# Performance work log

Measured on AMD Instinct MI355X. Metric: run time of the kernel, lower is better.

The kernel has to match this reference:

```python
import jax, jax.numpy as jnp
import numpy as np

N_NODES = 40000
N_EDGES = 1280000
D_FEAT = 1024
HIDDEN = 64
N_CLASSES = 40


def gcn_conv(x, edge_index, W, b):
    # PyG GCNConv: linear transform, add self-loops, symmetric deg^{-1/2} normalization, scatter-add
    n = x.shape[0]
    h = x @ W  # [N, out]
    loop = jnp.arange(n, dtype=edge_index.dtype)
    row = jnp.concatenate([edge_index[0], loop])  # source
    col = jnp.concatenate([edge_index[1], loop])  # target
    deg = jax.ops.segment_sum(jnp.ones_like(col, dtype=x.dtype), col, num_segments=n)
    dinv = jnp.where(deg > 0, jax.lax.rsqrt(deg), 0.0).astype(x.dtype)
    norm = dinv[row] * dinv[col]  # [E+N]
    msg = h[row] * norm[:, None]
    out = jax.ops.segment_sum(msg, col, num_segments=n)
    return out + b


def setup_inputs() -> dict:
    key = jax.random.key(0)
    k1, k2, k3, k4 = jax.random.split(key, 4)
    x = jax.random.normal(k1, (N_NODES, D_FEAT), dtype=jnp.float32)
    edge_index = jax.random.randint(k2, (2, N_EDGES), 0, N_NODES, dtype=jnp.int32)
    W1 = jax.random.normal(k3, (D_FEAT, HIDDEN), dtype=jnp.float32) * (1.0 / np.sqrt(D_FEAT))
    b1 = jnp.zeros((HIDDEN,), dtype=jnp.float32)
    W2 = jax.random.normal(k4, (HIDDEN, N_CLASSES), dtype=jnp.float32) * (1.0 / np.sqrt(HIDDEN))
    b2 = jnp.zeros((N_CLASSES,), dtype=jnp.float32)
    return {"x": x, "edge_index": edge_index, "W1": W1, "b1": b1, "W2": W2, "b2": b2}


def reference(x, edge_index, W1, b1, W2, b2):
    h = gcn_conv(x, edge_index, W1, b1)
    h = jax.nn.relu(h)
    # F.dropout(training=False) -> identity in eval mode
    h = gcn_conv(h, edge_index, W2, b2)
    return jax.nn.log_softmax(h, axis=1)
```

## Files before the change

### kernel.cpp

```cpp
#include <hip/hip_runtime.h>
#include <hip/hip_bf16.h>
#include <math.h>

#define N_NODES 40000
#define N_EDGES 1280000
#define D_FEAT 1024
#define HIDDEN 64
#define N_CLASSES 40
#define NB 157
#define CHUNK 8192

typedef _Float16 f16x8 __attribute__((ext_vector_type(8)));
typedef _Float16 f16x2 __attribute__((ext_vector_type(2)));
typedef float f32x4 __attribute__((ext_vector_type(4)));


__global__ __launch_bounds__(256) void k_binhist(const int* __restrict__ col,
                                                 int* __restrict__ btot) {
    __shared__ int h[NB];
    int tid = threadIdx.x;
    if (tid < NB) h[tid] = 0;
    __syncthreads();
    int e0 = blockIdx.x * 4096;
    int e1 = min(e0 + 4096, N_EDGES);
    for (int e = e0 + tid; e < e1; e += 256)
        atomicAdd(&h[col[e] >> 8], 1);
    __syncthreads();
    if (tid < NB && h[tid]) atomicAdd(&btot[tid], h[tid]);
}


__global__ __launch_bounds__(256) void k_bucketscan(const int* __restrict__ btot,
                                                    int* __restrict__ bucketBase,
                                                    int* __restrict__ bucketCursor) {
    __shared__ int s[256];
    int tid = threadIdx.x;
    int v = (tid < NB) ? btot[tid] : 0;
    s[tid] = v;
    __syncthreads();
#pragma unroll
    for (int d = 1; d < 256; d <<= 1) {
        int t = (tid >= d) ? s[tid - d] : 0;
        __syncthreads();
        s[tid] += t;
        __syncthreads();
    }
    int excl = s[tid] - v;
    if (tid < NB) { bucketBase[tid] = excl; bucketCursor[tid] = excl; }
    if (tid == 0) bucketBase[NB] = N_EDGES;
}


__global__ __launch_bounds__(256) void k_binscatter(const int* __restrict__ row,
                                                    const int* __restrict__ col,
                                                    int* __restrict__ bucketCursor,
                                                    uint2* __restrict__ sedge) {
    __shared__ int hist[NB];
    __shared__ int chunkBase[NB];
    __shared__ int cur[NB];
    int tid = threadIdx.x;
    int e0 = blockIdx.x * CHUNK;
    int e1 = min(e0 + CHUNK, N_EDGES);
    if (tid < NB) { hist[tid] = 0; cur[tid] = 0; }
    __syncthreads();
    for (int e = e0 + tid; e < e1; e += 256)
        atomicAdd(&hist[col[e] >> 8], 1);
    __syncthreads();
    if (tid < NB)
        chunkBase[tid] = hist[tid] ? atomicAdd(&bucketCursor[tid], hist[tid]) : 0;
    __syncthreads();
    for (int e = e0 + tid; e < e1; e += 256) {
        int c = col[e];
        int b = c >> 8;
        int p = atomicAdd(&cur[b], 1);
        sedge[chunkBase[b] + p] = make_uint2((unsigned)row[e], (unsigned)c);
    }
}


__global__ __launch_bounds__(256) void k_bucketsort(const uint2* __restrict__ sedge,
                                                    const int* __restrict__ bucketBase,
                                                    int* __restrict__ off,
                                                    float* __restrict__ dinv,
                                                    int* __restrict__ sorted) {
    __shared__ int hist[256];
    __shared__ int s[256];
    __shared__ int cur[256];
    int tid = threadIdx.x;
    int b = blockIdx.x;
    int base = bucketBase[b], end = bucketBase[b + 1];
    int col0 = b << 8;
    int ncol = min(256, N_NODES - col0);
    hist[tid] = 0;
    __syncthreads();
    for (int i = base + tid; i < end; i += 256)
        atomicAdd(&hist[sedge[i].y & 255], 1);
    __syncthreads();
    int v = hist[tid];
    s[tid] = v;
    __syncthreads();
#pragma unroll
    for (int d = 1; d < 256; d <<= 1) {
        int t = (tid >= d) ? s[tid - d] : 0;
        __syncthreads();
        s[tid] += t;
        __syncthreads();
    }
    int excl = s[tid] - v;
    cur[tid] = excl;
    if (tid < ncol) {
        off[col0 + tid] = base + excl;
        dinv[col0 + tid] = rsqrtf((float)(v + 1));
    }
    if (b == NB - 1 && tid == 0) off[N_NODES] = N_EDGES;
    __syncthreads();
    for (int i = base + tid; i < end; i += 256) {
        uint2 e = sedge[i];
        int p = atomicAdd(&cur[e.y & 255], 1);
        sorted[base + p] = (int)e.x;
    }
}


__global__ void k_convW1(const float* __restrict__ W, _Float16* __restrict__ Wt) {
    int i = blockIdx.x * 256 + threadIdx.x;
    if (i < D_FEAT * HIDDEN) {
        int n = i & 63, k = i >> 6;
        Wt[n * D_FEAT + k] = (_Float16)W[k * HIDDEN + n];
    }
}


#define LDA 72
#define LDB 72

__global__ __launch_bounds__(256) void k_gemm1(const float* __restrict__ X,
                                               const _Float16* __restrict__ Wt,
                                               const float* __restrict__ dinv,
                                               _Float16* __restrict__ out) {
    __shared__ _Float16 As[32 * LDA];
    __shared__ _Float16 Bs[64 * LDB];
    const int tid = threadIdx.x;
    const int wave = tid >> 6, lane = tid & 63;
    const int row0 = blockIdx.x * 32;
    const int m0 = (wave & 1) * 16, n0 = (wave >> 1) * 32;
    const int lr = lane & 15, quad = lane >> 4;

    const int ar = tid >> 3;
    const int ak = (tid & 7) * 8;
    const int bn = tid >> 2;
    const int bk = (tid & 3) * 16;

    f32x4 acc0 = {0.f, 0.f, 0.f, 0.f};
    f32x4 acc1 = {0.f, 0.f, 0.f, 0.f};

    for (int k0 = 0; k0 < D_FEAT; k0 += 64) {
        const float* xp = &X[(row0 + ar) * D_FEAT + k0 + ak];
        float4 v0 = *(const float4*)xp;
        float4 v1 = *(const float4*)(xp + 4);
        _Float16* ad = &As[ar * LDA + ak];
        ad[0] = (_Float16)v0.x; ad[1] = (_Float16)v0.y;
        ad[2] = (_Float16)v0.z; ad[3] = (_Float16)v0.w;
        ad[4] = (_Float16)v1.x; ad[5] = (_Float16)v1.y;
        ad[6] = (_Float16)v1.z; ad[7] = (_Float16)v1.w;
        const uint4* wp = (const uint4*)&Wt[bn * D_FEAT + k0 + bk];
        uint4 w0 = wp[0], w1 = wp[1];
        *(uint4*)&Bs[bn * LDB + bk] = w0;
        *(uint4*)&Bs[bn * LDB + bk + 8] = w1;
        __syncthreads();
#pragma unroll
        for (int kk = 0; kk < 64; kk += 32) {
            f16x8 a  = *(f16x8*)&As[(m0 + lr) * LDA + kk + quad * 8];
            f16x8 b0 = *(f16x8*)&Bs[(n0 + lr) * LDB + kk + quad * 8];
            f16x8 b1 = *(f16x8*)&Bs[(n0 + 16 + lr) * LDB + kk + quad * 8];
            acc0 = __builtin_amdgcn_mfma_f32_16x16x32_f16(a, b0, acc0, 0, 0, 0);
            acc1 = __builtin_amdgcn_mfma_f32_16x16x32_f16(a, b1, acc1, 0, 0, 0);
        }
        __syncthreads();
    }

#pragma unroll
    for (int r = 0; r < 4; ++r) {
        int m = row0 + m0 + quad * 4 + r;
        float dv = dinv[m];
        out[m * HIDDEN + n0 + lr]      = (_Float16)(acc0[r] * dv);
        out[m * HIDDEN + n0 + 16 + lr] = (_Float16)(acc1[r] * dv);
    }
}


__global__ __launch_bounds__(256) void k_gather1(const int* __restrict__ off,
                                                 const int* __restrict__ sorted,
                                                 const _Float16* __restrict__ hs,
                                                 const float* __restrict__ dinv,
                                                 const float* __restrict__ bias,
                                                 float* __restrict__ out) {
    int node = (blockIdx.x * 256 + threadIdx.x) >> 6;
    int lane = threadIdx.x & 63;
    if (node >= N_NODES) return;
    int h = lane >> 5, fl = lane & 31;
    float ax = 0.f, ay = 0.f;
    if (h == 0) {
        f16x2 v = *(const f16x2*)&hs[node * HIDDEN + 2 * fl];
        ax = (float)v.x; ay = (float)v.y;
    }
    int beg = off[node], end = off[node + 1];
    int j = beg + h;
    for (; j + 2 < end; j += 4) {
        int s0 = sorted[j], s1 = sorted[j + 2];
        f16x2 v0 = *(const f16x2*)&hs[s0 * HIDDEN + 2 * fl];
        f16x2 v1 = *(const f16x2*)&hs[s1 * HIDDEN + 2 * fl];
        ax += (float)v0.x + (float)v1.x;
        ay += (float)v0.y + (float)v1.y;
    }
    for (; j < end; j += 2) {
        int s = sorted[j];
        f16x2 v = *(const f16x2*)&hs[s * HIDDEN + 2 * fl];
        ax += (float)v.x; ay += (float)v.y;
    }
    ax += __shfl_xor(ax, 32, 64);
    ay += __shfl_xor(ay, 32, 64);
    if (h == 0) {
        float dv = dinv[node];
        float2 o;
        o.x = fmaxf(fmaf(dv, ax, bias[2 * fl + 0]), 0.f);
        o.y = fmaxf(fmaf(dv, ay, bias[2 * fl + 1]), 0.f);
        *(float2*)&out[node * HIDDEN + 2 * fl] = o;
    }
}


__global__ __launch_bounds__(256) void k_gemm2(const float* __restrict__ A,
                                               const float* __restrict__ W,
                                               const float* __restrict__ dinv,
                                               _Float16* __restrict__ out) {
    __shared__ float Ws[HIDDEN * N_CLASSES];
    __shared__ float Aa[32][65];
    const int tid = threadIdx.x;
    const int node0 = blockIdx.x * 32;

    for (int i = tid; i < HIDDEN * N_CLASSES; i += 256) Ws[i] = W[i];
    for (int i = tid * 4; i < 32 * HIDDEN; i += 1024) {
        float4 v = *(const float4*)&A[node0 * HIDDEN + i];
        int n = i >> 6, k = i & 63;
        Aa[n][k + 0] = v.x; Aa[n][k + 1] = v.y; Aa[n][k + 2] = v.z; Aa[n][k + 3] = v.w;
    }
    __syncthreads();

    const int n = tid >> 3;
    const int c0 = (tid & 7) * 5;
    float acc[5] = {};
#pragma unroll
    for (int k = 0; k < HIDDEN; ++k) {
        float av = Aa[n][k];
#pragma unroll
        for (int j = 0; j < 5; ++j) acc[j] += av * Ws[k * N_CLASSES + c0 + j];
    }
    float dv = dinv[node0 + n];
#pragma unroll
    for (int j = 0; j < 5; ++j)
        out[(node0 + n) * N_CLASSES + c0 + j] = (_Float16)(acc[j] * dv);
}


__global__ __launch_bounds__(256) void k_gather2_lsm(const int* __restrict__ off,
                                                     const int* __restrict__ sorted,
                                                     const _Float16* __restrict__ hs,
                                                     const float* __restrict__ dinv,
                                                     const float* __restrict__ bias,
                                                     float* __restrict__ out) {
    int node = (blockIdx.x * 256 + threadIdx.x) >> 6;
    int lane = threadIdx.x & 63;
    if (node >= N_NODES) return;
    int h = lane >> 5, fl = lane & 31;
    bool act = fl < 20;
    float ax = 0.f, ay = 0.f;
    if (h == 0 && act) {
        f16x2 v = *(const f16x2*)&hs[node * N_CLASSES + 2 * fl];
        ax = (float)v.x; ay = (float)v.y;
    }
    int beg = off[node], end = off[node + 1];
    int j = beg + h;
    for (; j + 2 < end; j += 4) {
        int s0 = sorted[j], s1 = sorted[j + 2];
        if (act) {
            f16x2 v0 = *(const f16x2*)&hs[s0 * N_CLASSES + 2 * fl];
            f16x2 v1 = *(const f16x2*)&hs[s1 * N_CLASSES + 2 * fl];
            ax += (float)v0.x + (float)v1.x;
            ay += (float)v0.y + (float)v1.y;
        }
    }
    for (; j < end; j += 2) {
        int s = sorted[j];
        if (act) {
            f16x2 v = *(const f16x2*)&hs[s * N_CLASSES + 2 * fl];
            ax += (float)v.x; ay += (float)v.y;
        }
    }
    ax += __shfl_xor(ax, 32, 64);
    ay += __shfl_xor(ay, 32, 64);
    float dv = dinv[node];
    float zx = act ? fmaf(dv, ax, bias[2 * fl + 0]) : -INFINITY;
    float zy = act ? fmaf(dv, ay, bias[2 * fl + 1]) : -INFINITY;
    float m = fmaxf(zx, zy);
#pragma unroll
    for (int d = 16; d > 0; d >>= 1) m = fmaxf(m, __shfl_xor(m, d, 64));
    float ex = act ? (expf(zx - m) + expf(zy - m)) : 0.f;
#pragma unroll
    for (int d = 16; d > 0; d >>= 1) ex += __shfl_xor(ex, d, 64);
    float lse = m + logf(ex);
    if (h == 0 && act) {
        float2 o; o.x = zx - lse; o.y = zy - lse;
        *(float2*)&out[node * N_CLASSES + 2 * fl] = o;
    }
}


extern "C" void kernel_launch(void* const* d_in, const int* in_sizes, int n_in,
                              void* d_out, int out_size, void* d_ws, size_t ws_size,
                              hipStream_t stream) {
    const float* x  = (const float*)d_in[0];
    const int*   ei = (const int*)d_in[1];
    const float* W1 = (const float*)d_in[2];
    const float* b1 = (const float*)d_in[3];
    const float* W2 = (const float*)d_in[4];
    const float* b2 = (const float*)d_in[5];
    const int* row = ei;
    const int* col = ei + N_EDGES;

    char* ws = (char*)d_ws;
    int*      btot         = (int*)(ws + 0);
    int*      bucketBase   = (int*)(ws + 1024);
    int*      bucketCursor = (int*)(ws + 2048);
    int*      off          = (int*)(ws + 4096);
    float*    dinv         = (float*)(ws + 172032);
    uint2*    sedge        = (uint2*)(ws + 335872);
    int*      sorted       = (int*)(ws + 10575872);
    _Float16* W1t          = (_Float16*)(ws + 15695872);
    _Float16* B1           = (_Float16*)(ws + 15826944);
    float*    B2           = (float*)(ws + 20946944);
    _Float16* B3           = (_Float16*)(ws + 31186944);

    hipMemsetAsync(btot, 0, NB * sizeof(int), stream);
    k_binhist<<<(N_EDGES + 4095) / 4096, 256, 0, stream>>>(col, btot);
    k_bucketscan<<<1, 256, 0, stream>>>(btot, bucketBase, bucketCursor);
    k_binscatter<<<(N_EDGES + CHUNK - 1) / CHUNK, 256, 0, stream>>>(row, col, bucketCursor, sedge);
    k_bucketsort<<<NB, 256, 0, stream>>>(sedge, bucketBase, off, dinv, sorted);

    k_convW1<<<(D_FEAT * HIDDEN) / 256, 256, 0, stream>>>(W1, W1t);
    k_gemm1<<<N_NODES / 32, 256, 0, stream>>>(x, W1t, dinv, B1);
    k_gather1<<<(N_NODES + 3) / 4, 256, 0, stream>>>(off, sorted, B1, dinv, b1, B2);

    k_gemm2<<<N_NODES / 32, 256, 0, stream>>>(B2, W2, dinv, B3);
    k_gather2_lsm<<<(N_NODES + 3) / 4, 256, 0, stream>>>(off, sorted, B3, dinv, b2, (float*)d_out);
}
```

Baseline: 427.3 us.

## Fuse layer-1 gather with layer-2 GEMM, merge prep kernels, widen GEMM1 tile

The histogram and W1 transpose kernels are merged into one launch. GEMM1 now computes 64 rows by all 64 output columns per block with wider vectorized loads. The layer-1 gather is fused with the 64x40 layer-2 matmul, which removes the fp32 intermediate round trip through global memory and one launch. Both gather loops are unrolled to 4 neighbours per iteration to raise memory-level parallelism. The fused kernel adds a per-block W2 shared-memory load and a block-wide sync that may cost occupancy.

```diff
diff --git a/kernel.cpp b/kernel.cpp
--- a/kernel.cpp
+++ b/kernel.cpp
@@ -15,18 +15,29 @@
 typedef float f32x4 __attribute__((ext_vector_type(4)));
 
 
-__global__ __launch_bounds__(256) void k_binhist(const int* __restrict__ col,
-                                                 int* __restrict__ btot) {
+#define HIST_BLOCKS 313
+#define CONV_BLOCKS 256
+
+__global__ __launch_bounds__(256) void k_pre(const int* __restrict__ col,
+                                             int* __restrict__ btot,
+                                             const float* __restrict__ W,
+                                             _Float16* __restrict__ Wt) {
     __shared__ int h[NB];
     int tid = threadIdx.x;
-    if (tid < NB) h[tid] = 0;
-    __syncthreads();
-    int e0 = blockIdx.x * 4096;
-    int e1 = min(e0 + 4096, N_EDGES);
-    for (int e = e0 + tid; e < e1; e += 256)
-        atomicAdd(&h[col[e] >> 8], 1);
-    __syncthreads();
-    if (tid < NB && h[tid]) atomicAdd(&btot[tid], h[tid]);
+    if (blockIdx.x < HIST_BLOCKS) {
+        if (tid < NB) h[tid] = 0;
+        __syncthreads();
+        int e0 = blockIdx.x * 4096;
+        int e1 = min(e0 + 4096, N_EDGES);
+        for (int e = e0 + tid; e < e1; e += 256)
+            atomicAdd(&h[col[e] >> 8], 1);
+        __syncthreads();
+        if (tid < NB && h[tid]) atomicAdd(&btot[tid], h[tid]);
+    } else {
+        int i = (blockIdx.x - HIST_BLOCKS) * 256 + tid;
+        int n = i & 63, k = i >> 6;
+        Wt[n * D_FEAT + k] = (_Float16)W[k * HIDDEN + n];
+    }
 }
 
 
@@ -122,15 +133,6 @@
 }
 
 
-__global__ void k_convW1(const float* __restrict__ W, _Float16* __restrict__ Wt) {
-    int i = blockIdx.x * 256 + threadIdx.x;
-    if (i < D_FEAT * HIDDEN) {
-        int n = i & 63, k = i >> 6;
-        Wt[n * D_FEAT + k] = (_Float16)W[k * HIDDEN + n];
-    }
-}
-
-
 #define LDA 72
 #define LDB 72
 
@@ -138,43 +140,48 @@
                                                const _Float16* __restrict__ Wt,
                                                const float* __restrict__ dinv,
                                                _Float16* __restrict__ out) {
-    __shared__ _Float16 As[32 * LDA];
+    __shared__ _Float16 As[64 * LDA];
     __shared__ _Float16 Bs[64 * LDB];
     const int tid = threadIdx.x;
     const int wave = tid >> 6, lane = tid & 63;
-    const int row0 = blockIdx.x * 32;
-    const int m0 = (wave & 1) * 16, n0 = (wave >> 1) * 32;
+    const int row0 = blockIdx.x * 64;
+    const int m0 = wave * 16;
     const int lr = lane & 15, quad = lane >> 4;
 
-    const int ar = tid >> 3;
-    const int ak = (tid & 7) * 8;
-    const int bn = tid >> 2;
-    const int bk = (tid & 3) * 16;
-
-    f32x4 acc0 = {0.f, 0.f, 0.f, 0.f};
-    f32x4 acc1 = {0.f, 0.f, 0.f, 0.f};
+    const int ar = tid >> 2;
+    const int ak = (tid & 3) * 16;
+
+    f32x4 acc0 = {0.f,0.f,0.f,0.f}, acc1 = {0.f,0.f,0.f,0.f};
+    f32x4 acc2 = {0.f,0.f,0.f,0.f}, acc3 = {0.f,0.f,0.f,0.f};
 
     for (int k0 = 0; k0 < D_FEAT; k0 += 64) {
         const float* xp = &X[(row0 + ar) * D_FEAT + k0 + ak];
-        float4 v0 = *(const float4*)xp;
+        float4 v0 = *(const float4*)(xp + 0);
         float4 v1 = *(const float4*)(xp + 4);
-        _Float16* ad = &As[ar * LDA + ak];
-        ad[0] = (_Float16)v0.x; ad[1] = (_Float16)v0.y;
-        ad[2] = (_Float16)v0.z; ad[3] = (_Float16)v0.w;
-        ad[4] = (_Float16)v1.x; ad[5] = (_Float16)v1.y;
-        ad[6] = (_Float16)v1.z; ad[7] = (_Float16)v1.w;
-        const uint4* wp = (const uint4*)&Wt[bn * D_FEAT + k0 + bk];
+        float4 v2 = *(const float4*)(xp + 8);
+        float4 v3 = *(const float4*)(xp + 12);
+        f16x8 p0 = {(_Float16)v0.x,(_Float16)v0.y,(_Float16)v0.z,(_Float16)v0.w,
+                    (_Float16)v1.x,(_Float16)v1.y,(_Float16)v1.z,(_Float16)v1.w};
+        f16x8 p1 = {(_Float16)v2.x,(_Float16)v2.y,(_Float16)v2.z,(_Float16)v2.w,
+                    (_Float16)v3.x,(_Float16)v3.y,(_Float16)v3.z,(_Float16)v3.w};
+        *(f16x8*)&As[ar * LDA + ak]     = p0;
+        *(f16x8*)&As[ar * LDA + ak + 8] = p1;
+        const uint4* wp = (const uint4*)&Wt[ar * D_FEAT + k0 + ak];
         uint4 w0 = wp[0], w1 = wp[1];
-        *(uint4*)&Bs[bn * LDB + bk] = w0;
-        *(uint4*)&Bs[bn * LDB + bk + 8] = w1;
+        *(uint4*)&Bs[ar * LDB + ak]     = w0;
+        *(uint4*)&Bs[ar * LDB + ak + 8] = w1;
         __syncthreads();
 #pragma unroll
         for (int kk = 0; kk < 64; kk += 32) {
             f16x8 a  = *(f16x8*)&As[(m0 + lr) * LDA + kk + quad * 8];
-            f16x8 b0 = *(f16x8*)&Bs[(n0 + lr) * LDB + kk + quad * 8];
-            f16x8 b1 = *(f16x8*)&Bs[(n0 + 16 + lr) * LDB + kk + quad * 8];
+            f16x8 b0 = *(f16x8*)&Bs[( 0 + lr) * LDB + kk + quad * 8];
+            f16x8 b1 = *(f16x8*)&Bs[(16 + lr) * LDB + kk + quad * 8];
+            f16x8 b2 = *(f16x8*)&Bs[(32 + lr) * LDB + kk + quad * 8];
+            f16x8 b3 = *(f16x8*)&Bs[(48 + lr) * LDB + kk + quad * 8];
             acc0 = __builtin_amdgcn_mfma_f32_16x16x32_f16(a, b0, acc0, 0, 0, 0);
             acc1 = __builtin_amdgcn_mfma_f32_16x16x32_f16(a, b1, acc1, 0, 0, 0);
+            acc2 = __builtin_amdgcn_mfma_f32_16x16x32_f16(a, b2, acc2, 0, 0, 0);
+            acc3 = __builtin_amdgcn_mfma_f32_16x16x32_f16(a, b3, acc3, 0, 0, 0);
         }
         __syncthreads();
     }
@@ -183,21 +190,30 @@
     for (int r = 0; r < 4; ++r) {
         int m = row0 + m0 + quad * 4 + r;
         float dv = dinv[m];
-        out[m * HIDDEN + n0 + lr]      = (_Float16)(acc0[r] * dv);
-        out[m * HIDDEN + n0 + 16 + lr] = (_Float16)(acc1[r] * dv);
-    }
-}
-
-
-__global__ __launch_bounds__(256) void k_gather1(const int* __restrict__ off,
-                                                 const int* __restrict__ sorted,
-                                                 const _Float16* __restrict__ hs,
-                                                 const float* __restrict__ dinv,
-                                                 const float* __restrict__ bias,
-                                                 float* __restrict__ out) {
-    int node = (blockIdx.x * 256 + threadIdx.x) >> 6;
-    int lane = threadIdx.x & 63;
-    if (node >= N_NODES) return;
+        out[m * HIDDEN +  0 + lr] = (_Float16)(acc0[r] * dv);
+        out[m * HIDDEN + 16 + lr] = (_Float16)(acc1[r] * dv);
+        out[m * HIDDEN + 32 + lr] = (_Float16)(acc2[r] * dv);
+        out[m * HIDDEN + 48 + lr] = (_Float16)(acc3[r] * dv);
+    }
+}
+
+
+__global__ __launch_bounds__(256) void k_g1g2(const int* __restrict__ off,
+                                              const int* __restrict__ sorted,
+                                              const _Float16* __restrict__ hs,
+                                              const float* __restrict__ dinv,
+                                              const float* __restrict__ bias,
+                                              const float* __restrict__ W2,
+                                              _Float16* __restrict__ B3) {
+    __shared__ float W2t[N_CLASSES][65];
+    __shared__ float a1s[4][64];
+    const int tid = threadIdx.x;
+    const int wave = tid >> 6, lane = tid & 63;
+    const int node = blockIdx.x * 4 + wave;
+
+    for (int i = tid; i < HIDDEN * N_CLASSES; i += 256)
+        W2t[i % N_CLASSES][i / N_CLASSES] = W2[i];
+
     int h = lane >> 5, fl = lane & 31;
     float ax = 0.f, ay = 0.f;
     if (h == 0) {
@@ -206,12 +222,14 @@
     }
     int beg = off[node], end = off[node + 1];
     int j = beg + h;
-    for (; j + 2 < end; j += 4) {
-        int s0 = sorted[j], s1 = sorted[j + 2];
+    for (; j + 6 < end; j += 8) {
+        int s0 = sorted[j], s1 = sorted[j + 2], s2 = sorted[j + 4], s3 = sorted[j + 6];
         f16x2 v0 = *(const f16x2*)&hs[s0 * HIDDEN + 2 * fl];
         f16x2 v1 = *(const f16x2*)&hs[s1 * HIDDEN + 2 * fl];
-        ax += (float)v0.x + (float)v1.x;
-        ay += (float)v0.y + (float)v1.y;
+        f16x2 v2 = *(const f16x2*)&hs[s2 * HIDDEN + 2 * fl];
+        f16x2 v3 = *(const f16x2*)&hs[s3 * HIDDEN + 2 * fl];
+        ax += (float)v0.x + (float)v1.x + (float)v2.x + (float)v3.x;
+        ay += (float)v0.y + (float)v1.y + (float)v2.y + (float)v3.y;
     }
     for (; j < end; j += 2) {
         int s = sorted[j];
@@ -220,46 +238,22 @@
     }
     ax += __shfl_xor(ax, 32, 64);
     ay += __shfl_xor(ay, 32, 64);
+    float dv = dinv[node];
     if (h == 0) {
-        float dv = dinv[node];
         float2 o;
         o.x = fmaxf(fmaf(dv, ax, bias[2 * fl + 0]), 0.f);
         o.y = fmaxf(fmaf(dv, ay, bias[2 * fl + 1]), 0.f);
-        *(float2*)&out[node * HIDDEN + 2 * fl] = o;
-    }
-}
-
-
-__global__ __launch_bounds__(256) void k_gemm2(const float* __restrict__ A,
-                                               const float* __restrict__ W,
-                                               const float* __restrict__ dinv,
-                                               _Float16* __restrict__ out) {
-    __shared__ float Ws[HIDDEN * N_CLASSES];
-    __shared__ float Aa[32][65];
-    const int tid = threadIdx.x;
-    const int node0 = blockIdx.x * 32;
-
-    for (int i = tid; i < HIDDEN * N_CLASSES; i += 256) Ws[i] = W[i];
-    for (int i = tid * 4; i < 32 * HIDDEN; i += 1024) {
-        float4 v = *(const float4*)&A[node0 * HIDDEN + i];
-        int n = i >> 6, k = i & 63;
-        Aa[n][k + 0] = v.x; Aa[n][k + 1] = v.y; Aa[n][k + 2] = v.z; Aa[n][k + 3] = v.w;
-    }
-    __syncthreads();
-
-    const int n = tid >> 3;
-    const int c0 = (tid & 7) * 5;
-    float acc[5] = {};
-#pragma unroll
-    for (int k = 0; k < HIDDEN; ++k) {
-        float av = Aa[n][k];
-#pragma unroll
-        for (int j = 0; j < 5; ++j) acc[j] += av * Ws[k * N_CLASSES + c0 + j];
-    }
-    float dv = dinv[node0 + n];
-#pragma unroll
-    for (int j = 0; j < 5; ++j)
-        out[(node0 + n) * N_CLASSES + c0 + j] = (_Float16)(acc[j] * dv);
+        *(float2*)&a1s[wave][2 * fl] = o;
+    }
+    __syncthreads();
+
+    if (lane < N_CLASSES) {
+        float acc = 0.f;
+#pragma unroll
+        for (int k = 0; k < HIDDEN; ++k)
+            acc = fmaf(a1s[wave][k], W2t[lane][k], acc);
+        B3[node * N_CLASSES + lane] = (_Float16)(acc * dv);
+    }
 }
 
 
@@ -281,13 +275,15 @@
     }
     int beg = off[node], end = off[node + 1];
     int j = beg + h;
-    for (; j + 2 < end; j += 4) {
-        int s0 = sorted[j], s1 = sorted[j + 2];
+    for (; j + 6 < end; j += 8) {
+        int s0 = sorted[j], s1 = sorted[j + 2], s2 = sorted[j + 4], s3 = sorted[j + 6];
         if (act) {
             f16x2 v0 = *(const f16x2*)&hs[s0 * N_CLASSES + 2 * fl];
             f16x2 v1 = *(const f16x2*)&hs[s1 * N_CLASSES + 2 * fl];
-            ax += (float)v0.x + (float)v1.x;
-            ay += (float)v0.y + (float)v1.y;
+            f16x2 v2 = *(const f16x2*)&hs[s2 * N_CLASSES + 2 * fl];
+            f16x2 v3 = *(const f16x2*)&hs[s3 * N_CLASSES + 2 * fl];
+            ax += (float)v0.x + (float)v1.x + (float)v2.x + (float)v3.x;
+            ay += (float)v0.y + (float)v1.y + (float)v2.y + (float)v3.y;
         }
     }
     for (; j < end; j += 2) {
@@ -338,19 +334,15 @@
     int*      sorted       = (int*)(ws + 10575872);
     _Float16* W1t          = (_Float16*)(ws + 15695872);
     _Float16* B1           = (_Float16*)(ws + 15826944);
-    float*    B2           = (float*)(ws + 20946944);
-    _Float16* B3           = (_Float16*)(ws + 31186944);
+    _Float16* B3           = (_Float16*)(ws + 20946944);
 
     hipMemsetAsync(btot, 0, NB * sizeof(int), stream);
-    k_binhist<<<(N_EDGES + 4095) / 4096, 256, 0, stream>>>(col, btot);
+    k_pre<<<HIST_BLOCKS + CONV_BLOCKS, 256, 0, stream>>>(col, btot, W1, W1t);
     k_bucketscan<<<1, 256, 0, stream>>>(btot, bucketBase, bucketCursor);
     k_binscatter<<<(N_EDGES + CHUNK - 1) / CHUNK, 256, 0, stream>>>(row, col, bucketCursor, sedge);
     k_bucketsort<<<NB, 256, 0, stream>>>(sedge, bucketBase, off, dinv, sorted);
 
-    k_convW1<<<(D_FEAT * HIDDEN) / 256, 256, 0, stream>>>(W1, W1t);
-    k_gemm1<<<N_NODES / 32, 256, 0, stream>>>(x, W1t, dinv, B1);
-    k_gather1<<<(N_NODES + 3) / 4, 256, 0, stream>>>(off, sorted, B1, dinv, b1, B2);
-
-    k_gemm2<<<N_NODES / 32, 256, 0, stream>>>(B2, W2, dinv, B3);
+    k_gemm1<<<N_NODES / 64, 256, 0, stream>>>(x, W1t, dinv, B1);
+    k_g1g2<<<N_NODES / 4, 256, 0, stream>>>(off, sorted, B1, dinv, b1, W2, B3);
     k_gather2_lsm<<<(N_NODES + 3) / 4, 256, 0, stream>>>(off, sorted, B3, dinv, b2, (float*)d_out);
 }
```

Result: faster. 409.8 us (-4.1%).
